# Optimization experiments

Measured on AMD Instinct MI355X. Metric: run time of the kernel, lower is better.

The kernel has to match this reference:

```python
import jax, jax.numpy as jnp
import numpy as np

B, T, D = 16, 4096, 256


def setup_inputs() -> dict:
    key = jax.random.key(0)
    ks = jax.random.split(key, 10)
    s = 1.0 / np.sqrt(D)  # torch nn.Linear default init range
    inp = {
        "x": jax.random.normal(ks[0], (B, T, D), jnp.float32),
        "hidden": jax.random.normal(ks[1], (B, D), jnp.float32),
    }
    names = ["W0", "b0", "W1", "b1", "W2", "b2", "W3", "b3"]
    for i, n in enumerate(names):
        shape = (D, D) if n.startswith("W") else (D,)
        inp[n] = jax.random.uniform(ks[2 + i], shape, jnp.float32, -s, s)
    return inp


def _gln(x, W0, b0, W1, b1, W2, b2, W3, b3):
    # Two gated-linear blocks; the final Linear(hyper[-1], hidden_size) in the
    # original module is never applied by calc_gln (index == len-1 is skipped).
    h = (x @ W0.T + b0) * jax.nn.sigmoid(x @ W1.T + b1)
    return (h @ W2.T + b2) * jax.nn.sigmoid(h @ W3.T + b3)


def reference(x, hidden, W0, b0, W1, b1, W2, b2, W3, b3):
    b = _gln(x, W0, b0, W1, b1, W2, b2, W3, b3)  # [B, T, D]
    bt = jnp.swapaxes(b, 0, 1)  # [T, B, D] for time-major scan
    init = jax.nn.relu(bt[0] + jnp.roll(hidden, 1, -1))

    def step(prev, b_t):
        out = jax.nn.relu(b_t + jnp.roll(prev, 1, -1))
        return out, out

    last, ys = jax.lax.scan(step, init, bt[1:])
    outputs = jnp.concatenate([init[None], ys], axis=0)  # [T, B, D]
    outputs = jnp.swapaxes(outputs, 0, 1)  # [B, T, D]; squeeze(2) is a no-op for D>1
    return outputs, last
```

## Files before the change

kernel.cpp:

```cpp
#include <hip/hip_runtime.h>
#include <hip/hip_bf16.h>
#include <cstdint>
#include <cstddef>

typedef __bf16 bf16x8 __attribute__((ext_vector_type(8)));
typedef float  f32x4  __attribute__((ext_vector_type(4)));

static constexpr int B  = 16;
static constexpr int T  = 4096;
static constexpr int D  = 256;
static constexpr int M  = B * T;
static constexpr int SEGS = 64;
static constexpr int SEGL = T / SEGS;

#define RBAR() do { asm volatile("" ::: "memory"); \
                    __builtin_amdgcn_s_barrier();  \
                    asm volatile("" ::: "memory"); } while (0)
#define LGKM0() asm volatile("s_waitcnt lgkmcnt(0)" ::: "memory")

__device__ __forceinline__ float sigmoid_fast(float v) {
    return __builtin_amdgcn_rcpf(1.0f + __expf(-v));
}

__global__ void cvt_w(const float* __restrict__ W0, const float* __restrict__ W1,
                      const float* __restrict__ W2, const float* __restrict__ W3,
                      __bf16* __restrict__ wp) {
    int i = blockIdx.x * blockDim.x + threadIdx.x;
    int s    = i >> 14;
    int r    = i & 16383;
    int ks   = r >> 11;
    int fg   = (r >> 6) & 31;
    int lane = r & 63;
    int kg = lane >> 4, rl = lane & 15;
    int w = fg >> 2, f = fg & 3;
    int q = f >> 1, gate = f & 1;
    int rc = w * 32 + 2 * rl + q;
    const float* src = (s == 0) ? (gate ? W1 : W0) : (gate ? W3 : W2);
    const float* p = src + (size_t)rc * 256 + ks * 32 + kg * 8;
    bf16x8 o;
#pragma unroll
    for (int j = 0; j < 8; ++j) o[j] = (__bf16)p[j];
    *reinterpret_cast<bf16x8*>(wp + (size_t)s * 131072 +
                               ((size_t)((ks * 32 + fg) * 64 + lane)) * 8) = o;
}

__launch_bounds__(512, 4)
__global__ void gln_fused(const float* __restrict__ x,
                          const __bf16* __restrict__ wp,
                          const float* __restrict__ b0, const float* __restrict__ b1,
                          const float* __restrict__ b2, const float* __restrict__ b3,
                          float* __restrict__ out,
                          float2* __restrict__ seg_am) {
    __shared__ char tile[32768];

    const int tid  = threadIdx.x;
    const int lane = tid & 63;
    const int wid  = tid >> 6;
    const int rl   = lane & 15;
    const int kg   = lane >> 4;
    const int row0 = blockIdx.x * 64;

    const __bf16* wv0 = wp + ((size_t)(wid * 4) * 64 + lane) * 8;
    const __bf16* wv1 = wv0 + 131072;

    bf16x8 bbuf[2][4];
    auto loadB = [&](int p, const __bf16* wvb, int ks) {
#pragma unroll
        for (int f = 0; f < 4; ++f)
            bbuf[p][f] = *reinterpret_cast<const bf16x8*>(wvb + ks * 16384 + f * 512);
    };

    {
        int r  = tid >> 3;
        int c0 = tid & 7;
        const float* xr = x + (size_t)(row0 + r) * 256;
        float4 xa[4][2];
#pragma unroll
        for (int ci = 0; ci < 4; ++ci) {
            const float4* p = reinterpret_cast<const float4*>(xr + (c0 + ci * 8) * 8);
            xa[ci][0] = p[0];
            xa[ci][1] = p[1];
        }
#pragma unroll
        for (int ci = 0; ci < 4; ++ci) {
            int ck = c0 + ci * 8;
            int pc = ck ^ ((r & 7) << 2);
            bf16x8 o = { (__bf16)xa[ci][0].x, (__bf16)xa[ci][0].y,
                         (__bf16)xa[ci][0].z, (__bf16)xa[ci][0].w,
                         (__bf16)xa[ci][1].x, (__bf16)xa[ci][1].y,
                         (__bf16)xa[ci][1].z, (__bf16)xa[ci][1].w };
            *reinterpret_cast<bf16x8*>(&tile[r * 512 + pc * 16]) = o;
        }
    }
    loadB(0, wv0, 0);
    LGKM0(); RBAR();

    f32x4 acc[4][4];

    auto run_stage = [&](const __bf16* wvb) {
#pragma unroll
        for (int m = 0; m < 4; ++m)
#pragma unroll
            for (int f = 0; f < 4; ++f) acc[m][f] = (f32x4){0.f, 0.f, 0.f, 0.f};
#pragma unroll
        for (int ks = 0; ks < 8; ++ks) {
            if (ks < 7) loadB((ks + 1) & 1, wvb, ks + 1);
            bf16x8 aR[4];
#pragma unroll
            for (int m = 0; m < 4; ++m) {
                int row = m * 16 + rl;
                int pc  = (ks * 4 + kg) ^ ((row & 7) << 2);
                aR[m] = *reinterpret_cast<const bf16x8*>(&tile[row * 512 + pc * 16]);
            }
#pragma unroll
            for (int m = 0; m < 4; ++m)
#pragma unroll
                for (int f = 0; f < 4; ++f)
                    acc[m][f] = __builtin_amdgcn_mfma_f32_16x16x32_bf16(
                        aR[m], bbuf[ks & 1][f], acc[m][f], 0, 0, 0);
        }
    };

    const int rc0 = wid * 32 + 2 * rl;

    run_stage(wv0);
    loadB(0, wv1, 0);
    RBAR();
    {
        float2 bb0 = *reinterpret_cast<const float2*>(b0 + rc0);
        float2 bb1 = *reinterpret_cast<const float2*>(b1 + rc0);
        int cb  = rc0 * 2;
        int ck  = cb >> 4;
        int off = cb & 15;
#pragma unroll
        for (int m = 0; m < 4; ++m)
#pragma unroll
            for (int j = 0; j < 4; ++j) {
                int row = m * 16 + kg * 4 + j;
                float he = (acc[m][0][j] + bb0.x) * sigmoid_fast(acc[m][1][j] + bb1.x);
                float ho = (acc[m][2][j] + bb0.y) * sigmoid_fast(acc[m][3][j] + bb1.y);
                unsigned short ue = __builtin_bit_cast(unsigned short, (__bf16)he);
                unsigned short uo = __builtin_bit_cast(unsigned short, (__bf16)ho);
                unsigned int u = ((unsigned int)uo << 16) | (unsigned int)ue;
                int pc = ck ^ ((row & 7) << 2);
                *reinterpret_cast<unsigned int*>(&tile[row * 512 + pc * 16 + off]) = u;
            }
    }
    LGKM0(); RBAR();

    run_stage(wv1);

    float2 ov[16];
    {
        float2 bb2 = *reinterpret_cast<const float2*>(b2 + rc0);
        float2 bb3 = *reinterpret_cast<const float2*>(b3 + rc0);
#pragma unroll
        for (int m = 0; m < 4; ++m)
#pragma unroll
            for (int j = 0; j < 4; ++j) {
                float he = (acc[m][0][j] + bb2.x) * sigmoid_fast(acc[m][1][j] + bb3.x);
                float ho = (acc[m][2][j] + bb2.y) * sigmoid_fast(acc[m][3][j] + bb3.y);
                float2 o; o.x = he; o.y = ho;
                ov[m * 4 + j] = o;
            }
    }
    RBAR();

    float* ftile = reinterpret_cast<float*>(tile);
#pragma unroll
    for (int m = 0; m < 2; ++m)
#pragma unroll
        for (int j = 0; j < 4; ++j) {
            int row = m * 16 + kg * 4 + j;
            int col = rc0 ^ ((row & 7) << 2);
            *reinterpret_cast<float2*>(&ftile[row * 256 + col]) = ov[m * 4 + j];
        }
    LGKM0(); RBAR();

    const int batch = row0 >> 12;
    const int t0    = row0 & 4095;
    const int seg   = t0 >> 6;
    float A = 0.f, Mx = -1e30f;
    int cc = 0;
    if (tid < 256) {
        cc = (tid + t0) & 255;
#pragma unroll 8
        for (int i = 0; i < 32; ++i) {
            int col = ((cc + i) & 255) ^ ((i & 7) << 2);
            float v = ftile[i * 256 + col];
            A += v;
            Mx = fmaxf(Mx + v, 0.f);
        }
    }
    RBAR();
#pragma unroll
    for (int m = 2; m < 4; ++m)
#pragma unroll
        for (int j = 0; j < 4; ++j) {
            int row = m * 16 + kg * 4 + j;
            int pr  = row & 31;
            int col = rc0 ^ ((pr & 7) << 2);
            *reinterpret_cast<float2*>(&ftile[pr * 256 + col]) = ov[m * 4 + j];
        }

#pragma unroll
    for (int m = 0; m < 4; ++m)
#pragma unroll
        for (int j = 0; j < 4; ++j) {
            int row = m * 16 + kg * 4 + j;
            *reinterpret_cast<float2*>(out + (size_t)(row0 + row) * 256 + rc0) =
                ov[m * 4 + j];
        }
    LGKM0(); RBAR();

    if (tid < 256) {
#pragma unroll 8
        for (int i = 32; i < 64; ++i) {
            int pr  = i - 32;
            int col = ((cc + i) & 255) ^ ((pr & 7) << 2);
            float v = ftile[pr * 256 + col];
            A += v;
            Mx = fmaxf(Mx + v, 0.f);
        }
        float2 o; o.x = A; o.y = Mx;
        seg_am[(size_t)(batch * SEGS + seg) * 256 + tid] = o;
    }
}

__global__ void scan_apply(float* __restrict__ bio,
                           const float2* __restrict__ seg_am,
                           const float* __restrict__ hidden,
                           float* __restrict__ last) {
    int tid   = blockIdx.x * blockDim.x + threadIdx.x;
    int c     = tid & 255;
    int rest  = tid >> 8;
    int batch = rest & 15;
    int seg   = rest >> 4;
    float s = hidden[batch * 256 + ((c + 255) & 255)];
    const float2* am = seg_am + ((size_t)batch * SEGS) * 256 + c;
    for (int k = 0; k < seg; ++k) {
        float2 a = am[(size_t)k * 256];
        s = fmaxf(s + a.x, a.y);
    }
    float* base = bio + (size_t)batch * T * D;
    int t0 = seg * SEGL;
#pragma unroll 8
    for (int i = 0; i < SEGL; ++i) {
        int t = t0 + i;
        size_t idx = (size_t)t * 256 + ((c + t) & 255);
        float v = base[idx];
        s = fmaxf(s + v, 0.f);
        base[idx] = s;
    }
    if (seg == SEGS - 1) last[batch * 256 + ((c + 255) & 255)] = s;
}

extern "C" void kernel_launch(void* const* d_in, const int* in_sizes, int n_in,
                              void* d_out, int out_size, void* d_ws, size_t ws_size,
                              hipStream_t stream) {
    const float* x      = (const float*)d_in[0];
    const float* hidden = (const float*)d_in[1];
    const float* W0 = (const float*)d_in[2];
    const float* b0 = (const float*)d_in[3];
    const float* W1 = (const float*)d_in[4];
    const float* b1 = (const float*)d_in[5];
    const float* W2 = (const float*)d_in[6];
    const float* b2 = (const float*)d_in[7];
    const float* W3 = (const float*)d_in[8];
    const float* b3 = (const float*)d_in[9];

    float* out  = (float*)d_out;
    float* last = out + (size_t)M * D;

    char* ws = (char*)d_ws;
    __bf16* wpb    = (__bf16*)ws;
    float2* seg_am = (float2*)(ws + 524288);

    cvt_w<<<128, 256, 0, stream>>>(W0, W1, W2, W3, wpb);
    gln_fused<<<M / 64, 512, 0, stream>>>(x, wpb, b0, b1, b2, b3, out, seg_am);
    scan_apply<<<(B * D * SEGS) / 256, 256, 0, stream>>>(out, seg_am, hidden, last);
}
```

Before: 84.09 us.

## Stage weight slices into LDS via async global_load_lds triple buffering

Weights were previously loaded straight from global memory into registers, with double buffering per wave. They are now streamed through a three-slot LDS ring using global_load_lds, gated by vmcnt waits and barriers, and both GEMM stages run as one 16-iteration loop. This is meant to hide weight-load latency and let the block share weight fetches through LDS. In exchange each block now takes 128KB of dynamic LDS and launch bounds drop to 2 blocks per CU, which lowers occupancy and adds a barrier to every iteration.

```diff
diff --git a/kernel.cpp b/kernel.cpp
--- a/kernel.cpp
+++ b/kernel.cpp
@@ -5,6 +5,9 @@
 
 typedef __bf16 bf16x8 __attribute__((ext_vector_type(8)));
 typedef float  f32x4  __attribute__((ext_vector_type(4)));
+
+#define AS1 __attribute__((address_space(1)))
+#define AS3 __attribute__((address_space(3)))
 
 static constexpr int B  = 16;
 static constexpr int T  = 4096;
@@ -17,6 +20,8 @@
                     __builtin_amdgcn_s_barrier();  \
                     asm volatile("" ::: "memory"); } while (0)
 #define LGKM0() asm volatile("s_waitcnt lgkmcnt(0)" ::: "memory")
+#define VMCNT4() asm volatile("s_waitcnt vmcnt(4)" ::: "memory")
+#define VMCNT0() asm volatile("s_waitcnt vmcnt(0)" ::: "memory")
 
 __device__ __forceinline__ float sigmoid_fast(float v) {
     return __builtin_amdgcn_rcpf(1.0f + __expf(-v));
@@ -44,14 +49,15 @@
                                ((size_t)((ks * 32 + fg) * 64 + lane)) * 8) = o;
 }
 
-__launch_bounds__(512, 4)
+__launch_bounds__(512, 2)
 __global__ void gln_fused(const float* __restrict__ x,
                           const __bf16* __restrict__ wp,
                           const float* __restrict__ b0, const float* __restrict__ b1,
                           const float* __restrict__ b2, const float* __restrict__ b3,
                           float* __restrict__ out,
                           float2* __restrict__ seg_am) {
-    __shared__ char tile[32768];
+    extern __shared__ char smem[];
+    char* tile = smem;
 
     const int tid  = threadIdx.x;
     const int lane = tid & 63;
@@ -59,16 +65,12 @@
     const int rl   = lane & 15;
     const int kg   = lane >> 4;
     const int row0 = blockIdx.x * 64;
-
-    const __bf16* wv0 = wp + ((size_t)(wid * 4) * 64 + lane) * 8;
-    const __bf16* wv1 = wv0 + 131072;
-
-    bf16x8 bbuf[2][4];
-    auto loadB = [&](int p, const __bf16* wvb, int ks) {
-#pragma unroll
-        for (int f = 0; f < 4; ++f)
-            bbuf[p][f] = *reinterpret_cast<const bf16x8*>(wvb + ks * 16384 + f * 512);
-    };
+    const int rc0  = wid * 32 + 2 * rl;
+
+    float2 bb0 = *reinterpret_cast<const float2*>(b0 + rc0);
+    float2 bb1 = *reinterpret_cast<const float2*>(b1 + rc0);
+    float2 bb2 = *reinterpret_cast<const float2*>(b2 + rc0);
+    float2 bb3 = *reinterpret_cast<const float2*>(b3 + rc0);
 
     {
         int r  = tid >> 3;
@@ -92,78 +94,89 @@
             *reinterpret_cast<bf16x8*>(&tile[r * 512 + pc * 16]) = o;
         }
     }
-    loadB(0, wv0, 0);
-    LGKM0(); RBAR();
+
+    auto issueSlice = [&](int si) {
+        const char* src = reinterpret_cast<const char*>(wp) + (size_t)si * 32768;
+        char* dst = smem + 32768 + (si % 3) * 32768;
+#pragma unroll
+        for (int ld = 0; ld < 4; ++ld) {
+            int ch = ld * 512 + tid;
+            __builtin_amdgcn_global_load_lds(
+                (const AS1 void*)(src + (size_t)ch * 16),
+                (AS3 void*)(dst + (size_t)ch * 16), 16, 0, 0);
+        }
+    };
+    issueSlice(0);
+    issueSlice(1);
+    LGKM0();
 
     f32x4 acc[4][4];
-
-    auto run_stage = [&](const __bf16* wvb) {
+#pragma unroll
+    for (int m = 0; m < 4; ++m)
+#pragma unroll
+        for (int f = 0; f < 4; ++f) acc[m][f] = (f32x4){0.f, 0.f, 0.f, 0.f};
+
+#pragma unroll
+    for (int it = 0; it < 16; ++it) {
+        if (it < 15) { VMCNT4(); } else { VMCNT0(); }
+        RBAR();
+
+        if (it == 8) {
+            int cb  = rc0 * 2;
+            int ck  = cb >> 4;
+            int off = cb & 15;
+#pragma unroll
+            for (int m = 0; m < 4; ++m)
+#pragma unroll
+                for (int j = 0; j < 4; ++j) {
+                    int row = m * 16 + kg * 4 + j;
+                    float he = (acc[m][0][j] + bb0.x) * sigmoid_fast(acc[m][1][j] + bb1.x);
+                    float ho = (acc[m][2][j] + bb0.y) * sigmoid_fast(acc[m][3][j] + bb1.y);
+                    unsigned short ue = __builtin_bit_cast(unsigned short, (__bf16)he);
+                    unsigned short uo = __builtin_bit_cast(unsigned short, (__bf16)ho);
+                    unsigned int u = ((unsigned int)uo << 16) | (unsigned int)ue;
+                    int pc = ck ^ ((row & 7) << 2);
+                    *reinterpret_cast<unsigned int*>(&tile[row * 512 + pc * 16 + off]) = u;
+                }
+            LGKM0(); RBAR();
+#pragma unroll
+            for (int m = 0; m < 4; ++m)
+#pragma unroll
+                for (int f = 0; f < 4; ++f) acc[m][f] = (f32x4){0.f, 0.f, 0.f, 0.f};
+        }
+
+        const int ks = it & 7;
+        const char* wb = smem + 32768 + (it % 3) * 32768;
+        bf16x8 bR[4], aR[4];
+#pragma unroll
+        for (int f = 0; f < 4; ++f)
+            bR[f] = *reinterpret_cast<const bf16x8*>(
+                wb + ((size_t)((wid * 4 + f) * 64 + lane)) * 16);
+#pragma unroll
+        for (int m = 0; m < 4; ++m) {
+            int row = m * 16 + rl;
+            int pc  = (ks * 4 + kg) ^ ((row & 7) << 2);
+            aR[m] = *reinterpret_cast<const bf16x8*>(&tile[row * 512 + pc * 16]);
+        }
+        if (it < 14) issueSlice(it + 2);
 #pragma unroll
         for (int m = 0; m < 4; ++m)
 #pragma unroll
-            for (int f = 0; f < 4; ++f) acc[m][f] = (f32x4){0.f, 0.f, 0.f, 0.f};
-#pragma unroll
-        for (int ks = 0; ks < 8; ++ks) {
-            if (ks < 7) loadB((ks + 1) & 1, wvb, ks + 1);
-            bf16x8 aR[4];
-#pragma unroll
-            for (int m = 0; m < 4; ++m) {
-                int row = m * 16 + rl;
-                int pc  = (ks * 4 + kg) ^ ((row & 7) << 2);
-                aR[m] = *reinterpret_cast<const bf16x8*>(&tile[row * 512 + pc * 16]);
-            }
-#pragma unroll
-            for (int m = 0; m < 4; ++m)
-#pragma unroll
-                for (int f = 0; f < 4; ++f)
-                    acc[m][f] = __builtin_amdgcn_mfma_f32_16x16x32_bf16(
-                        aR[m], bbuf[ks & 1][f], acc[m][f], 0, 0, 0);
-        }
-    };
-
-    const int rc0 = wid * 32 + 2 * rl;
-
-    run_stage(wv0);
-    loadB(0, wv1, 0);
-    RBAR();
-    {
-        float2 bb0 = *reinterpret_cast<const float2*>(b0 + rc0);
-        float2 bb1 = *reinterpret_cast<const float2*>(b1 + rc0);
-        int cb  = rc0 * 2;
-        int ck  = cb >> 4;
-        int off = cb & 15;
-#pragma unroll
-        for (int m = 0; m < 4; ++m)
-#pragma unroll
-            for (int j = 0; j < 4; ++j) {
-                int row = m * 16 + kg * 4 + j;
-                float he = (acc[m][0][j] + bb0.x) * sigmoid_fast(acc[m][1][j] + bb1.x);
-                float ho = (acc[m][2][j] + bb0.y) * sigmoid_fast(acc[m][3][j] + bb1.y);
-                unsigned short ue = __builtin_bit_cast(unsigned short, (__bf16)he);
-                unsigned short uo = __builtin_bit_cast(unsigned short, (__bf16)ho);
-                unsigned int u = ((unsigned int)uo << 16) | (unsigned int)ue;
-                int pc = ck ^ ((row & 7) << 2);
-                *reinterpret_cast<unsigned int*>(&tile[row * 512 + pc * 16 + off]) = u;
-            }
-    }
-    LGKM0(); RBAR();
-
-    run_stage(wv1);
+            for (int f = 0; f < 4; ++f)
+                acc[m][f] = __builtin_amdgcn_mfma_f32_16x16x32_bf16(
+                    aR[m], bR[f], acc[m][f], 0, 0, 0);
+    }
 
     float2 ov[16];
-    {
-        float2 bb2 = *reinterpret_cast<const float2*>(b2 + rc0);
-        float2 bb3 = *reinterpret_cast<const float2*>(b3 + rc0);
-#pragma unroll
-        for (int m = 0; m < 4; ++m)
-#pragma unroll
-            for (int j = 0; j < 4; ++j) {
-                float he = (acc[m][0][j] + bb2.x) * sigmoid_fast(acc[m][1][j] + bb3.x);
-                float ho = (acc[m][2][j] + bb2.y) * sigmoid_fast(acc[m][3][j] + bb3.y);
-                float2 o; o.x = he; o.y = ho;
-                ov[m * 4 + j] = o;
-            }
-    }
+#pragma unroll
+    for (int m = 0; m < 4; ++m)
+#pragma unroll
+        for (int j = 0; j < 4; ++j) {
+            float he = (acc[m][0][j] + bb2.x) * sigmoid_fast(acc[m][1][j] + bb3.x);
+            float ho = (acc[m][2][j] + bb2.y) * sigmoid_fast(acc[m][3][j] + bb3.y);
+            float2 o; o.x = he; o.y = ho;
+            ov[m * 4 + j] = o;
+        }
     RBAR();
 
     float* ftile = reinterpret_cast<float*>(tile);
@@ -276,7 +289,14 @@
     __bf16* wpb    = (__bf16*)ws;
     float2* seg_am = (float2*)(ws + 524288);
 
+    static bool attr_done = false;
+    if (!attr_done) {
+        hipFuncSetAttribute(reinterpret_cast<const void*>(&gln_fused),
+                            hipFuncAttributeMaxDynamicSharedMemorySize, 131072);
+        attr_done = true;
+    }
+
     cvt_w<<<128, 256, 0, stream>>>(W0, W1, W2, W3, wpb);
-    gln_fused<<<M / 64, 512, 0, stream>>>(x, wpb, b0, b1, b2, b3, out, seg_am);
+    gln_fused<<<M / 64, 512, 131072, stream>>>(x, wpb, b0, b1, b2, b3, out, seg_am);
     scan_apply<<<(B * D * SEGS) / 256, 256, 0, stream>>>(out, seg_am, hidden, last);
 }
```

After: 95.54 us. +13.6%, slower.
